# Optimization experiments

Measured on AMD Instinct MI355X. Metric: run time of the kernel, lower is better.

Reference implementation:

```python
import jax, jax.numpy as jnp
import numpy as np
from functools import partial

NUM_QUERIES = 900
TOPK_PRE = 100      # topk(100) in source
TOPK_POST = 20      # keep_inds[:20] in source
IOU_THR = 0.7


def cxcywh_to_xyxy(b):
    cx, cy, w, h = b[..., 0], b[..., 1], b[..., 2], b[..., 3]
    return jnp.stack([cx - 0.5 * w, cy - 0.5 * h, cx + 0.5 * w, cy + 0.5 * h], axis=-1)


def nms_single(boxes, scores):
    # boxes: [K,4] xyxy, already sorted by descending score (top_k output).
    # Single class per patch in this module, so batched_nms == plain nms.
    K = boxes.shape[0]
    area = jnp.clip(boxes[:, 2] - boxes[:, 0], 0) * jnp.clip(boxes[:, 3] - boxes[:, 1], 0)
    lt = jnp.maximum(boxes[:, None, :2], boxes[None, :, :2])
    rb = jnp.minimum(boxes[:, None, 2:], boxes[None, :, 2:])
    wh = jnp.clip(rb - lt, 0)
    inter = wh[..., 0] * wh[..., 1]
    iou = inter / (area[:, None] + area[None, :] - inter + 1e-7)  # [K,K]
    idx = jnp.arange(K)

    def body(i, keep):
        sup = (iou[i] > IOU_THR) & (idx > i) & keep[i]
        return keep & (~sup)

    keep = jax.lax.fori_loop(0, K, body, jnp.ones((K,), bool))
    rank = jnp.cumsum(keep) - 1
    valid = keep & (rank < TOPK_POST)
    slot = jnp.where(valid, rank, TOPK_POST)  # invalid entries scatter into dropped slot
    sel_s = jnp.zeros((TOPK_POST + 1,), scores.dtype).at[slot].set(jnp.where(valid, scores, 0.0))[:TOPK_POST]
    sel_b = jnp.zeros((TOPK_POST + 1, 4), boxes.dtype).at[slot].set(jnp.where(valid[:, None], boxes, 0.0))[:TOPK_POST]
    vmask = jnp.zeros((TOPK_POST + 1,), bool).at[slot].set(valid)[:TOPK_POST]
    return sel_s, sel_b, vmask


def setup_inputs() -> dict:
    key = jax.random.key(0)
    k1, k2, k3, k4 = jax.random.split(key, 4)
    BS, P, Q, C = 16, 64, NUM_QUERIES, 2
    pred_logits = jax.random.normal(k1, (BS, 1, P * Q, C), jnp.float32)
    pred_boxes = jax.random.uniform(k2, (BS, 1, P * Q, 4), jnp.float32, minval=0.05, maxval=0.6)
    target_sizes = jax.random.uniform(k3, (BS, 2), jnp.float32, minval=480.0, maxval=1333.0)  # (h, w)
    labels = jax.random.randint(k4, (BS, P), 0, 80, jnp.int32)
    return {"pred_logits": pred_logits, "pred_boxes": pred_boxes,
            "target_sizes": target_sizes, "labels": labels}


def reference(pred_logits, pred_boxes, target_sizes, labels):
    BS = pred_logits.shape[0]
    Q = NUM_QUERIES
    score = jax.nn.sigmoid(pred_logits[:, 0, :, -1])          # [BS, N]
    boxes = cxcywh_to_xyxy(pred_boxes[:, 0])                   # [BS, N, 4]
    img_h, img_w = target_sizes[:, 0], target_sizes[:, 1]
    scale = jnp.stack([img_w, img_h, img_w, img_h], axis=-1)   # [BS, 4]
    boxes = boxes * scale[:, None, :]
    P = score.shape[1] // Q
    score = score.reshape(BS, P, Q)
    boxes = boxes.reshape(BS, P, Q, 4)
    top_s, top_i = jax.lax.top_k(score, TOPK_PRE)              # [BS, P, 100]
    top_b = jnp.take_along_axis(boxes, top_i[..., None], axis=2)  # [BS, P, 100, 4]
    sel_s, sel_b, vmask = jax.vmap(nms_single)(
        top_b.reshape(BS * P, TOPK_PRE, 4), top_s.reshape(BS * P, TOPK_PRE))
    sel_s = sel_s.reshape(BS, P, TOPK_POST)
    sel_b = sel_b.reshape(BS, P, TOPK_POST, 4)
    vmask = vmask.reshape(BS, P, TOPK_POST)
    sel_l = jnp.where(vmask, labels[:, :, None], -1)
    return sel_s, sel_b, sel_l, vmask
```

## Files before the change

### kernel.cpp

```cpp
#include <hip/hip_runtime.h>
#include <stdint.h>

#define NQ 900
#define TOPK_PRE 100
#define TOPK_POST 20
#define IOU_THR 0.7f
#define THREADS 256

typedef unsigned long long u64;

__device__ __forceinline__ u64 umin64(u64 a, u64 b) { return a < b ? a : b; }
__device__ __forceinline__ u64 umax64(u64 a, u64 b) { return a > b ? a : b; }


__global__ __launch_bounds__(THREADS)
void ovnms_kernel(const float* __restrict__ logits,
                  const float* __restrict__ boxes,
                  const float* __restrict__ tsize,
                  const int*   __restrict__ labels,
                  float* __restrict__ out)
{
#pragma clang fp contract(off)
    const int row  = blockIdx.x;
    const int b    = row >> 6;
    const int p    = row & 63;
    const int tid  = threadIdx.x;
    const int lane = tid & 63;
    const int wid  = tid >> 6;

    __shared__ u64 wl[4 * 128];
    __shared__ u64 md[2 * 128];
    __shared__ u64 fin[128];
    __shared__ u64 sup0[TOPK_PRE], sup1[TOPK_PRE];
    __shared__ float x1s[TOPK_PRE], y1s[TOPK_PRE], x2s[TOPK_PRE], y2s[TOPK_PRE];
    __shared__ float areas[TOPK_PRE], scs[TOPK_PRE];
    __shared__ u64 keep0s, keep1s;

    const float2* l2 = (const float2*)(logits + ((size_t)b * 57600 + (size_t)p * NQ) * 2);
    u64 kr[4];
#pragma unroll
    for (int r = 0; r < 4; ++r) {
        int q = wid * 64 + lane + r * 256;
        u64 key = ~0ull;
        if (q < NQ) {
            float x = l2[q].y;
            float s = 1.0f / (1.0f + expf(-x));
            unsigned u = __float_as_uint(s);
            key = ((u64)(~u) << 32) | (unsigned)q;
        }
        kr[r] = key;
    }

#pragma unroll
    for (int k = 2; k <= 256; k <<= 1) {
#pragma unroll
        for (int j = k >> 1; j > 0; j >>= 1) {
            if (j >= 64) {
                const int jr = j >> 6;
#pragma unroll
                for (int r = 0; r < 4; ++r) {
                    if ((r & jr) == 0) {
                        const int rp = r | jr;
                        bool up = (((r * 64) & k) == 0);
                        u64 lo = umin64(kr[r], kr[rp]);
                        u64 hi = umax64(kr[r], kr[rp]);
                        kr[r]  = up ? lo : hi;
                        kr[rp] = up ? hi : lo;
                    }
                }
            } else {
#pragma unroll
                for (int r = 0; r < 4; ++r) {
                    bool up = (((r * 64 + lane) & k) == 0);
                    u64 part = __shfl_xor(kr[r], j);
                    bool lower = ((lane & j) == 0);
                    kr[r] = (up == lower) ? umin64(kr[r], part) : umax64(kr[r], part);
                }
            }
        }
    }

    wl[wid * 128 + lane]      = kr[0];
    wl[wid * 128 + 64 + lane] = kr[1];
    __syncthreads();

    if (wid < 2) {
        const u64* A = &wl[(2 * wid) * 128];
        const u64* B = &wl[(2 * wid + 1) * 128];
        u64 c0 = umin64(A[lane],      B[127 - lane]);
        u64 c1 = umin64(A[64 + lane], B[63 - lane]);
        u64 lo = umin64(c0, c1), hi = umax64(c0, c1);
        c0 = lo; c1 = hi;
#pragma unroll
        for (int j = 32; j > 0; j >>= 1) {
            bool lower = (lane & j) == 0;
            u64 p0 = __shfl_xor(c0, j);
            u64 p1 = __shfl_xor(c1, j);
            c0 = lower ? umin64(c0, p0) : umax64(c0, p0);
            c1 = lower ? umin64(c1, p1) : umax64(c1, p1);
        }
        md[wid * 128 + lane]      = c0;
        md[wid * 128 + 64 + lane] = c1;
    }
    __syncthreads();

    if (wid == 0) {
        const u64* A = md;
        const u64* B = md + 128;
        u64 c0 = umin64(A[lane],      B[127 - lane]);
        u64 c1 = umin64(A[64 + lane], B[63 - lane]);
        u64 lo = umin64(c0, c1), hi = umax64(c0, c1);
        c0 = lo; c1 = hi;
#pragma unroll
        for (int j = 32; j > 0; j >>= 1) {
            bool lower = (lane & j) == 0;
            u64 p0 = __shfl_xor(c0, j);
            u64 p1 = __shfl_xor(c1, j);
            c0 = lower ? umin64(c0, p0) : umax64(c0, p0);
            c1 = lower ? umin64(c1, p1) : umax64(c1, p1);
        }
        fin[lane]      = c0;
        fin[64 + lane] = c1;
    }
    __syncthreads();

    if (tid < TOPK_PRE) {
        u64 key = fin[tid];
        int q = (int)(key & 0xFFFFFFFFu);
        scs[tid] = __uint_as_float(~(unsigned)(key >> 32));
        const float* brow = boxes + ((size_t)b * 57600 + (size_t)p * NQ + (size_t)q) * 4;
        float cx = brow[0], cy = brow[1], w = brow[2], h = brow[3];
        float ih = tsize[b * 2 + 0];
        float iw = tsize[b * 2 + 1];
        float xa = (cx - 0.5f * w) * iw;
        float ya = (cy - 0.5f * h) * ih;
        float xb = (cx + 0.5f * w) * iw;
        float yb = (cy + 0.5f * h) * ih;
        x1s[tid] = xa; y1s[tid] = ya; x2s[tid] = xb; y2s[tid] = yb;
        areas[tid] = fmaxf(xb - xa, 0.0f) * fmaxf(yb - ya, 0.0f);
    }
    __syncthreads();

    {
        const float xj1a = x1s[lane], yj1a = y1s[lane];
        const float xj2a = x2s[lane], yj2a = y2s[lane], aja = areas[lane];
        const int  j2   = lane + 64;
        const bool hv2  = j2 < TOPK_PRE;
        const int  j2c  = hv2 ? j2 : 0;
        const float xj1b = x1s[j2c], yj1b = y1s[j2c];
        const float xj2b = x2s[j2c], yj2b = y2s[j2c], ajb = areas[j2c];

#pragma unroll 5
        for (int i = wid; i < TOPK_PRE; i += 4) {
            float xi1 = x1s[i], yi1 = y1s[i], xi2 = x2s[i], yi2 = y2s[i], ai = areas[i];
            bool b0 = false;
            if (lane < i) {
                float ltx = fmaxf(xi1, xj1a);
                float lty = fmaxf(yi1, yj1a);
                float rbx = fminf(xi2, xj2a);
                float rby = fminf(yi2, yj2a);
                float wx = fmaxf(rbx - ltx, 0.0f);
                float wy = fmaxf(rby - lty, 0.0f);
                float inter = wx * wy;
                float iou = inter / (((ai + aja) - inter) + 1e-7f);
                b0 = iou > IOU_THR;
            }
            u64 m0 = __ballot(b0);
            bool b1 = false;
            if (hv2 && j2 < i) {
                float ltx = fmaxf(xi1, xj1b);
                float lty = fmaxf(yi1, yj1b);
                float rbx = fminf(xi2, xj2b);
                float rby = fminf(yi2, yj2b);
                float wx = fmaxf(rbx - ltx, 0.0f);
                float wy = fmaxf(rby - lty, 0.0f);
                float inter = wx * wy;
                float iou = inter / (((ai + ajb) - inter) + 1e-7f);
                b1 = iou > IOU_THR;
            }
            u64 m1 = __ballot(b1);
            if (lane == 0) { sup0[i] = m0; sup1[i] = m1; }
        }
    }
    __syncthreads();

    if (wid == 0) {
        u64 r0a = sup0[lane];
        u64 r1a = sup1[lane];
        const int  j2  = lane + 64;
        const bool hv2 = j2 < TOPK_PRE;
        u64 r0b = hv2 ? sup0[j2] : 0ull;
        u64 r1b = hv2 ? sup1[j2] : 0ull;
        bool alive_a = true;
        bool alive_b = hv2;

#pragma unroll 4
        for (int i = 0; i < 64; ++i) {
            u64 bal = __ballot(alive_a);
            if ((bal >> i) & 1ull) {
                alive_a = alive_a && !((r0a >> i) & 1ull);
                alive_b = alive_b && !((r0b >> i) & 1ull);
            }
        }
#pragma unroll 4
        for (int i = 64; i < TOPK_PRE; ++i) {
            u64 bal = __ballot(alive_b);
            if ((bal >> (i - 64)) & 1ull) {
                alive_a = alive_a && !((r1a >> (i - 64)) & 1ull);
                alive_b = alive_b && !((r1b >> (i - 64)) & 1ull);
            }
        }
        u64 B0 = __ballot(alive_a);
        u64 B1 = __ballot(alive_b);
        if (lane == 0) { keep0s = B0; keep1s = B1; }
    }
    __syncthreads();

    if (tid < TOPK_POST) {
        u64 K0 = keep0s, K1 = keep1s;
        int c0 = __popcll(K0);
        int idx = -1;
        if (tid < c0) {
            u64 x = K0;
            for (int k = 0; k < tid; ++k) x &= x - 1;
            idx = __ffsll(x) - 1;
        } else {
            int t = tid - c0;
            if (t < __popcll(K1)) {
                u64 x = K1;
                for (int k = 0; k < t; ++k) x &= x - 1;
                idx = 64 + __ffsll(x) - 1;
            }
        }
        size_t o = (size_t)row * TOPK_POST + (size_t)tid;
        float s = 0.0f, xa = 0.0f, ya = 0.0f, xb = 0.0f, yb = 0.0f;
        float lab = -1.0f, m = 0.0f;
        if (idx >= 0) {
            s = scs[idx];
            xa = x1s[idx]; ya = y1s[idx]; xb = x2s[idx]; yb = y2s[idx];
            lab = (float)labels[row];
            m = 1.0f;
        }
        out[o] = s;
        float* ob = out + 20480 + o * 4;
        ob[0] = xa; ob[1] = ya; ob[2] = xb; ob[3] = yb;
        out[102400 + o] = lab;
        out[122880 + o] = m;
    }
}

extern "C" void kernel_launch(void* const* d_in, const int* in_sizes, int n_in,
                              void* d_out, int out_size, void* d_ws, size_t ws_size,
                              hipStream_t stream) {
    const float* logits = (const float*)d_in[0];
    const float* boxes  = (const float*)d_in[1];
    const float* tsize  = (const float*)d_in[2];
    const int*   labels = (const int*)d_in[3];
    float* out = (float*)d_out;

    ovnms_kernel<<<dim3(1024), dim3(THREADS), 0, stream>>>(logits, boxes, tsize, labels, out);
}
```

Measured before the change: 37.07 us.

## Double block to 512 threads, sort 128 keys per wave, add merge level

Raises the block size from 256 to 512 threads so each of 8 waves loads and bitonic-sorts 128 keys (two registers) instead of 4 waves sorting 256 keys each. A third LDS merge level is added, and the IoU suppression loop now strides over 8 waves. The aim is to shorten the per-wave serial sort work and spread IoU rows over more waves, at the cost of an extra merge stage with a barrier and lower occupancy per block.

```diff
diff --git a/kernel.cpp b/kernel.cpp
--- a/kernel.cpp
+++ b/kernel.cpp
@@ -5,12 +5,35 @@
 #define TOPK_PRE 100
 #define TOPK_POST 20
 #define IOU_THR 0.7f
-#define THREADS 256
+#define THREADS 512
 
 typedef unsigned long long u64;
 
 __device__ __forceinline__ u64 umin64(u64 a, u64 b) { return a < b ? a : b; }
 __device__ __forceinline__ u64 umax64(u64 a, u64 b) { return a > b ? a : b; }
+
+__device__ __forceinline__ void ce(u64& v, int j, bool up, int lane) {
+    u64 part = __shfl_xor(v, j);
+    bool lower = ((lane & j) == 0);
+    v = (up == lower) ? umin64(v, part) : umax64(v, part);
+}
+
+__device__ __forceinline__ void merge_lds(const u64* __restrict__ A,
+                                          const u64* __restrict__ B,
+                                          u64& c0, u64& c1, int lane) {
+    c0 = umin64(A[lane],      B[127 - lane]);
+    c1 = umin64(A[64 + lane], B[63 - lane]);
+    u64 lo = umin64(c0, c1), hi = umax64(c0, c1);
+    c0 = lo; c1 = hi;
+#pragma unroll
+    for (int j = 32; j > 0; j >>= 1) {
+        bool lower = (lane & j) == 0;
+        u64 p0 = __shfl_xor(c0, j);
+        u64 p1 = __shfl_xor(c1, j);
+        c0 = lower ? umin64(c0, p0) : umax64(c0, p0);
+        c1 = lower ? umin64(c1, p1) : umax64(c1, p1);
+    }
+}
 
 
 __global__ __launch_bounds__(THREADS)
@@ -28,99 +51,75 @@
     const int lane = tid & 63;
     const int wid  = tid >> 6;
 
-    __shared__ u64 wl[4 * 128];
-    __shared__ u64 md[2 * 128];
+    __shared__ u64 wl[8 * 128];
+    __shared__ u64 md[4 * 128];
+    __shared__ u64 m2[2 * 128];
     __shared__ u64 fin[128];
-    __shared__ u64 sup0[TOPK_PRE], sup1[TOPK_PRE];
     __shared__ float x1s[TOPK_PRE], y1s[TOPK_PRE], x2s[TOPK_PRE], y2s[TOPK_PRE];
     __shared__ float areas[TOPK_PRE], scs[TOPK_PRE];
+    __shared__ u64 sup0[TOPK_PRE], sup1[TOPK_PRE];
     __shared__ u64 keep0s, keep1s;
 
-    const float2* l2 = (const float2*)(logits + ((size_t)b * 57600 + (size_t)p * NQ) * 2);
-    u64 kr[4];
-#pragma unroll
-    for (int r = 0; r < 4; ++r) {
-        int q = wid * 64 + lane + r * 256;
-        u64 key = ~0ull;
-        if (q < NQ) {
-            float x = l2[q].y;
+    const float* lrow = logits + ((size_t)b * 57600 + (size_t)p * NQ) * 2;
+    u64 c0, c1;
+    {
+        int q0 = wid * 128 + lane;
+        int q1 = q0 + 64;
+        u64 k0 = ~0ull, k1 = ~0ull;
+        if (q0 < NQ) {
+            float x = lrow[q0 * 2 + 1];
             float s = 1.0f / (1.0f + expf(-x));
-            unsigned u = __float_as_uint(s);
-            key = ((u64)(~u) << 32) | (unsigned)q;
-        }
-        kr[r] = key;
-    }
-
-#pragma unroll
-    for (int k = 2; k <= 256; k <<= 1) {
+            k0 = ((u64)(~__float_as_uint(s)) << 32) | (unsigned)q0;
+        }
+        if (q1 < NQ) {
+            float x = lrow[q1 * 2 + 1];
+            float s = 1.0f / (1.0f + expf(-x));
+            k1 = ((u64)(~__float_as_uint(s)) << 32) | (unsigned)q1;
+        }
+        c0 = k0; c1 = k1;
+    }
+
+#pragma unroll
+    for (int k = 2; k <= 64; k <<= 1) {
 #pragma unroll
         for (int j = k >> 1; j > 0; j >>= 1) {
-            if (j >= 64) {
-                const int jr = j >> 6;
-#pragma unroll
-                for (int r = 0; r < 4; ++r) {
-                    if ((r & jr) == 0) {
-                        const int rp = r | jr;
-                        bool up = (((r * 64) & k) == 0);
-                        u64 lo = umin64(kr[r], kr[rp]);
-                        u64 hi = umax64(kr[r], kr[rp]);
-                        kr[r]  = up ? lo : hi;
-                        kr[rp] = up ? hi : lo;
-                    }
-                }
-            } else {
-#pragma unroll
-                for (int r = 0; r < 4; ++r) {
-                    bool up = (((r * 64 + lane) & k) == 0);
-                    u64 part = __shfl_xor(kr[r], j);
-                    bool lower = ((lane & j) == 0);
-                    kr[r] = (up == lower) ? umin64(kr[r], part) : umax64(kr[r], part);
-                }
-            }
-        }
-    }
-
-    wl[wid * 128 + lane]      = kr[0];
-    wl[wid * 128 + 64 + lane] = kr[1];
-    __syncthreads();
-
-    if (wid < 2) {
-        const u64* A = &wl[(2 * wid) * 128];
-        const u64* B = &wl[(2 * wid + 1) * 128];
-        u64 c0 = umin64(A[lane],      B[127 - lane]);
-        u64 c1 = umin64(A[64 + lane], B[63 - lane]);
+            ce(c0, j, (lane & k) == 0, lane);
+            ce(c1, j, ((64 + lane) & k) == 0, lane);
+        }
+    }
+    {
         u64 lo = umin64(c0, c1), hi = umax64(c0, c1);
         c0 = lo; c1 = hi;
 #pragma unroll
         for (int j = 32; j > 0; j >>= 1) {
-            bool lower = (lane & j) == 0;
-            u64 p0 = __shfl_xor(c0, j);
-            u64 p1 = __shfl_xor(c1, j);
-            c0 = lower ? umin64(c0, p0) : umax64(c0, p0);
-            c1 = lower ? umin64(c1, p1) : umax64(c1, p1);
-        }
-        md[wid * 128 + lane]      = c0;
-        md[wid * 128 + 64 + lane] = c1;
-    }
-    __syncthreads();
-
+            ce(c0, j, true, lane);
+            ce(c1, j, true, lane);
+        }
+    }
+
+    wl[wid * 128 + lane]      = c0;
+    wl[wid * 128 + 64 + lane] = c1;
+    __syncthreads();
+
+    if (wid < 4) {
+        u64 a0, a1;
+        merge_lds(&wl[(2 * wid) * 128], &wl[(2 * wid + 1) * 128], a0, a1, lane);
+        md[wid * 128 + lane]      = a0;
+        md[wid * 128 + 64 + lane] = a1;
+    }
+    __syncthreads();
+    if (wid < 2) {
+        u64 a0, a1;
+        merge_lds(&md[(2 * wid) * 128], &md[(2 * wid + 1) * 128], a0, a1, lane);
+        m2[wid * 128 + lane]      = a0;
+        m2[wid * 128 + 64 + lane] = a1;
+    }
+    __syncthreads();
     if (wid == 0) {
-        const u64* A = md;
-        const u64* B = md + 128;
-        u64 c0 = umin64(A[lane],      B[127 - lane]);
-        u64 c1 = umin64(A[64 + lane], B[63 - lane]);
-        u64 lo = umin64(c0, c1), hi = umax64(c0, c1);
-        c0 = lo; c1 = hi;
-#pragma unroll
-        for (int j = 32; j > 0; j >>= 1) {
-            bool lower = (lane & j) == 0;
-            u64 p0 = __shfl_xor(c0, j);
-            u64 p1 = __shfl_xor(c1, j);
-            c0 = lower ? umin64(c0, p0) : umax64(c0, p0);
-            c1 = lower ? umin64(c1, p1) : umax64(c1, p1);
-        }
-        fin[lane]      = c0;
-        fin[64 + lane] = c1;
+        u64 a0, a1;
+        merge_lds(m2, m2 + 128, a0, a1, lane);
+        fin[lane]      = a0;
+        fin[64 + lane] = a1;
     }
     __syncthreads();
 
@@ -150,8 +149,8 @@
         const float xj1b = x1s[j2c], yj1b = y1s[j2c];
         const float xj2b = x2s[j2c], yj2b = y2s[j2c], ajb = areas[j2c];
 
-#pragma unroll 5
-        for (int i = wid; i < TOPK_PRE; i += 4) {
+#pragma unroll 4
+        for (int i = wid; i < TOPK_PRE; i += 8) {
             float xi1 = x1s[i], yi1 = y1s[i], xi2 = x2s[i], yi2 = y2s[i], ai = areas[i];
             bool b0 = false;
             if (lane < i) {
@@ -218,14 +217,14 @@
 
     if (tid < TOPK_POST) {
         u64 K0 = keep0s, K1 = keep1s;
-        int c0 = __popcll(K0);
+        int c0n = __popcll(K0);
         int idx = -1;
-        if (tid < c0) {
+        if (tid < c0n) {
             u64 x = K0;
             for (int k = 0; k < tid; ++k) x &= x - 1;
             idx = __ffsll(x) - 1;
         } else {
-            int t = tid - c0;
+            int t = tid - c0n;
             if (t < __popcll(K1)) {
                 u64 x = K1;
                 for (int k = 0; k < t; ++k) x &= x - 1;
```

Measured after the change: 34.42 us. 1.08x faster.
